# Kernel optimization log

Hardware: AMD Instinct MI355X
Metric: run time of the kernel (lower is better)

Reference implementation:

```python
import jax, jax.numpy as jnp
import numpy as np

B, C, H, W = 256, 3, 224, 224
RETINA = 32
NUM_ZOOM = 3
SCALE = 2
HG, HL = 1024, 256  # num_hidden_glimpse, num_hidden_location
GDIM = NUM_ZOOM * C * RETINA * RETINA  # 9216


def setup_inputs() -> dict:
    key = jax.random.key(0)
    ks = jax.random.split(key, 12)
    images = jax.random.normal(ks[0], (B, C, H, W), dtype=jnp.float32)
    # locations in [-0.4, 0.4] so all multi-scale crops are in-bounds
    locations = (jax.random.uniform(ks[1], (B, 2), dtype=jnp.float32) * 2.0 - 1.0) * 0.4
    def lin(kw, kb, fan_in, fan_out):
        s = 1.0 / np.sqrt(fan_in)
        Wm = jax.random.uniform(kw, (fan_in, fan_out), jnp.float32, -s, s)
        bm = jax.random.uniform(kb, (fan_out,), jnp.float32, -s, s)
        return Wm, bm
    W1, b1 = lin(ks[2], ks[3], GDIM, HG)
    W2, b2 = lin(ks[4], ks[5], 2, HL)
    W3, b3 = lin(ks[6], ks[7], HG, HG + HL)
    W4, b4 = lin(ks[8], ks[9], HL, HG + HL)
    return {"images": images, "locations": locations,
            "W1": W1, "b1": b1, "W2": W2, "b2": b2,
            "W3": W3, "b3": b3, "W4": W4, "b4": b4}


def _foveate(images, locations):
    # images (B,C,H,W); locations (B,2) in [-1,1]
    denorm = (locations + 1.0) * 0.5 * W  # denormalized pixel coords (row, col)
    zoom_patches = []
    for i in range(NUM_ZOOM):
        half = int(RETINA * 0.5 * SCALE ** i)
        size = 2 * half
        def crop(img, loc):
            # int() truncation == floor for in-bounds (non-negative) offsets
            top = jnp.trunc(loc[0] - half).astype(jnp.int32)
            left = jnp.trunc(loc[1] - half).astype(jnp.int32)
            return jax.lax.dynamic_slice(img, (jnp.int32(0), top, left), (C, size, size))
        crops = jax.vmap(crop)(images, denorm)  # (B,C,size,size)
        resized = jax.image.resize(crops, (crops.shape[0], C, RETINA, RETINA),
                                   method="bilinear", antialias=False)
        zoom_patches.append(resized)
    g = jnp.stack(zoom_patches, axis=1)  # (B, Z, C, r, r)
    return g.reshape(g.shape[0], -1)  # (B, Z*C*r*r)


def reference(images, locations, W1, b1, W2, b2, W3, b3, W4, b4):
    g = _foveate(images, locations)
    hg = jax.nn.relu(jax.nn.relu(g @ W1 + b1) @ W3 + b3)
    hl = jax.nn.relu(jax.nn.relu(locations @ W2 + b2) @ W4 + b4)
    return jax.nn.relu(hg + hl)
```

## Files before the change

kernel.cpp:

```cpp
#include <hip/hip_runtime.h>

typedef __attribute__((ext_vector_type(8))) short short8;
typedef __attribute__((ext_vector_type(16))) float f32x16;

#define Bsz 256
#define Cch 3
#define Him 224
#define Wim 224
#define RET 32
#define HG 1024
#define HL 256
#define GDIM 9216
#define NOUT 1280

__device__ __forceinline__ unsigned short f2bf(float x) {
  unsigned u = __float_as_uint(x);
  return (unsigned short)((u + 0x7fffu + ((u >> 16) & 1u)) >> 16);
}
__device__ __forceinline__ float bf2f(unsigned short h) {
  return __uint_as_float((unsigned)h << 16);
}

__global__ __launch_bounds__(256) void foveate_kernel(
    const float* __restrict__ img, const float* __restrict__ loc,
    unsigned short* __restrict__ ghi, unsigned short* __restrict__ glo) {
  int idx = blockIdx.x * 256 + threadIdx.x;
  int b = idx / GDIM;
  int r = idx - b * GDIM;
  int z = r / (Cch * RET * RET);
  int r2 = r - z * (Cch * RET * RET);
  int c = r2 / (RET * RET);
  int p = r2 - c * (RET * RET);
  int i = p >> 5, j = p & 31;
  float dr = (loc[b * 2 + 0] + 1.f) * .5f * (float)Wim;
  float dc = (loc[b * 2 + 1] + 1.f) * .5f * (float)Wim;
  int half = 16 << z;
  int top = (int)truncf(dr - (float)half), left = (int)truncf(dc - (float)half);
  const float* base = img + ((long)b * Cch + c) * (Him * Wim);
  float v;
  if (z == 0) {
    v = base[(top + i) * Wim + left + j];
  } else {
    int rr = (z == 1) ? top + 2 * i : top + 4 * i + 1;
    int cc = (z == 1) ? left + 2 * j : left + 4 * j + 1;
    v = .25f * (base[rr * Wim + cc] + base[rr * Wim + cc + 1] +
                base[(rr + 1) * Wim + cc] + base[(rr + 1) * Wim + cc + 1]);
  }
  unsigned short h = f2bf(v);
  ghi[idx] = h;
  glo[idx] = f2bf(v - bf2f(h));
}

__device__ __forceinline__ void gemm_block(
    const unsigned short* __restrict__ Ahi, const unsigned short* __restrict__ Alo,
    int lda, const float* __restrict__ Bf, int ldb,
    int m0, int n0, int kb, int iters,
    f32x16 acc[2][2], unsigned short* __restrict__ ldsA, float* __restrict__ ldsB) {
  const int t = threadIdx.x;
  const int lane = t & 63;
  const int wm = t >> 7, wn = (t >> 6) & 1;
  const int l5 = lane & 31, lh = lane >> 5;

  const unsigned short* aSrc[4];
  const float* bSrc[4];
  int aDst[4], bDst[4];
#pragma unroll
  for (int p = 0; p < 4; ++p) {
    int s = p * 256 + t;
    int m5 = s & 31, kseg = (s >> 5) & 3, mf = (s >> 7) & 3;
    const unsigned short* base = (s >> 9) ? Alo : Ahi;
    aSrc[p] = base + (long)(m0 + mf * 32 + m5) * lda + kb + kseg * 8;
    aDst[p] = s * 8;
    bSrc[p] = Bf + (long)(kb + (s & 1023) / 32) * ldb + n0 + (s & 31) * 4;
    bDst[p] = ((s & 1023) >> 5) * 128 + (s & 31) * 4;
  }

  for (int it = 0; it < iters; ++it) {
    uint4 av[4];
    float4 bv[4];
#pragma unroll
    for (int p = 0; p < 4; ++p) {
      av[p] = *(const uint4*)(aSrc[p] + it * 32);
      bv[p] = *(const float4*)(bSrc[p] + (long)it * 32 * ldb);
    }
    __syncthreads();
#pragma unroll
    for (int p = 0; p < 4; ++p) {
      *(uint4*)(ldsA + aDst[p]) = av[p];
      *(float4*)(ldsB + bDst[p]) = bv[p];
    }
    __syncthreads();
#pragma unroll
    for (int ks = 0; ks < 2; ++ks) {
      short8 ah[2], al[2], bh[2], bl[2];
#pragma unroll
      for (int mi = 0; mi < 2; ++mi) {
        int mf = wm * 2 + mi;
        int slot = mf * 128 + (ks * 2 + lh) * 32 + l5;
        ah[mi] = *(const short8*)(ldsA + slot * 8);
        al[mi] = *(const short8*)(ldsA + (slot + 512) * 8);
      }
#pragma unroll
      for (int ni = 0; ni < 2; ++ni) {
        int n = wn * 64 + ni * 32 + l5;
        int k0 = ks * 16 + lh * 8;
        short8 hh, ll;
#pragma unroll
        for (int j = 0; j < 8; ++j) {
          float v = ldsB[(k0 + j) * 128 + n];
          unsigned short h = f2bf(v);
          hh[j] = (short)h;
          ll[j] = (short)f2bf(v - bf2f(h));
        }
        bh[ni] = hh;
        bl[ni] = ll;
      }
#pragma unroll
      for (int mi = 0; mi < 2; ++mi)
#pragma unroll
        for (int ni = 0; ni < 2; ++ni) {
          acc[mi][ni] = __builtin_amdgcn_mfma_f32_32x32x16_bf16(ah[mi], bh[ni], acc[mi][ni], 0, 0, 0);
          acc[mi][ni] = __builtin_amdgcn_mfma_f32_32x32x16_bf16(ah[mi], bl[ni], acc[mi][ni], 0, 0, 0);
          acc[mi][ni] = __builtin_amdgcn_mfma_f32_32x32x16_bf16(al[mi], bh[ni], acc[mi][ni], 0, 0, 0);
        }
    }
  }
}

__device__ __forceinline__ void epilogue(float* __restrict__ Pz, int ldp, int m0,
                                         int n0, f32x16 acc[2][2]) {
  const int t = threadIdx.x, lane = t & 63;
  const int wm = t >> 7, wn = (t >> 6) & 1;
  const int l5 = lane & 31, lh = lane >> 5;
#pragma unroll
  for (int mi = 0; mi < 2; ++mi)
#pragma unroll
    for (int ni = 0; ni < 2; ++ni) {
      int col = n0 + wn * 64 + ni * 32 + l5;
      int rbase = m0 + wm * 64 + mi * 32 + 4 * lh;
#pragma unroll
      for (int r = 0; r < 16; ++r) {
        int row = rbase + (r & 3) + 8 * (r >> 2);
        Pz[(long)row * ldp + col] = acc[mi][ni][r];
      }
    }
}

__global__ __launch_bounds__(256, 2) void gemm1_kernel(
    const unsigned short* __restrict__ ghi, const unsigned short* __restrict__ glo,
    const float* __restrict__ W1, float* __restrict__ P) {
  __shared__ __align__(16) unsigned short ldsA[8192];
  __shared__ __align__(16) float ldsB[4096];
  f32x16 zz = {0, 0, 0, 0, 0, 0, 0, 0, 0, 0, 0, 0, 0, 0, 0, 0};
  f32x16 acc[2][2] = {zz, zz, zz, zz};
  int n0 = blockIdx.x * 128, m0 = blockIdx.y * 128, z = blockIdx.z;
  gemm_block(ghi, glo, GDIM, W1, HG, m0, n0, z * 288, 9, acc, ldsA, ldsB);
  epilogue(P + (long)z * Bsz * HG, HG, m0, n0, acc);
}

__global__ __launch_bounds__(256, 2) void gemm2_kernel(
    const unsigned short* __restrict__ h1hi, const unsigned short* __restrict__ h1lo,
    const unsigned short* __restrict__ h2hi, const unsigned short* __restrict__ h2lo,
    const float* __restrict__ W3, const float* __restrict__ W4,
    float* __restrict__ P) {
  __shared__ __align__(16) unsigned short ldsA[8192];
  __shared__ __align__(16) float ldsB[4096];
  f32x16 zz = {0, 0, 0, 0, 0, 0, 0, 0, 0, 0, 0, 0, 0, 0, 0, 0};
  f32x16 acc[2][2] = {zz, zz, zz, zz};
  int n0 = blockIdx.x * 128, m0 = blockIdx.y * 128, z = blockIdx.z;
  if (z < 8)
    gemm_block(h1hi, h1lo, HG, W3, NOUT, m0, n0, z * 128, 4, acc, ldsA, ldsB);
  else
    gemm_block(h2hi, h2lo, HL, W4, NOUT, m0, n0, (z - 8) * 128, 4, acc, ldsA, ldsB);
  epilogue(P + (long)z * Bsz * NOUT, NOUT, m0, n0, acc);
}

__global__ __launch_bounds__(256) void reduce1_h2_kernel(
    const float* __restrict__ P, const float* __restrict__ b1,
    const float* __restrict__ loc, const float* __restrict__ W2,
    const float* __restrict__ b2,
    unsigned short* __restrict__ h1hi, unsigned short* __restrict__ h1lo,
    unsigned short* __restrict__ h2hi, unsigned short* __restrict__ h2lo) {
  if (blockIdx.x < 256) {
    int i4 = (blockIdx.x * 256 + threadIdx.x) * 4;
    float4 s = *(const float4*)(P + i4);
    for (int z = 1; z < 32; ++z) {
      float4 p = *(const float4*)(P + (long)z * (Bsz * HG) + i4);
      s.x += p.x; s.y += p.y; s.z += p.z; s.w += p.w;
    }
    int n = i4 & (HG - 1);
    float4 bb = *(const float4*)(b1 + n);
    float v0 = fmaxf(s.x + bb.x, 0.f), v1 = fmaxf(s.y + bb.y, 0.f);
    float v2 = fmaxf(s.z + bb.z, 0.f), v3 = fmaxf(s.w + bb.w, 0.f);
    unsigned short h0 = f2bf(v0), h1 = f2bf(v1), h2 = f2bf(v2), h3 = f2bf(v3);
    *(ushort4*)(h1hi + i4) = make_ushort4(h0, h1, h2, h3);
    *(ushort4*)(h1lo + i4) = make_ushort4(f2bf(v0 - bf2f(h0)), f2bf(v1 - bf2f(h1)),
                                          f2bf(v2 - bf2f(h2)), f2bf(v3 - bf2f(h3)));
  } else {
    int i4 = ((blockIdx.x - 256) * 256 + threadIdx.x) * 4;
    int b = i4 >> 8, n = i4 & (HL - 1);
    float l0 = loc[b * 2 + 0], l1 = loc[b * 2 + 1];
    float4 w0 = *(const float4*)(W2 + n);
    float4 w1 = *(const float4*)(W2 + HL + n);
    float4 bb = *(const float4*)(b2 + n);
    float v0 = fmaxf(fmaf(l0, w0.x, fmaf(l1, w1.x, bb.x)), 0.f);
    float v1 = fmaxf(fmaf(l0, w0.y, fmaf(l1, w1.y, bb.y)), 0.f);
    float v2 = fmaxf(fmaf(l0, w0.z, fmaf(l1, w1.z, bb.z)), 0.f);
    float v3 = fmaxf(fmaf(l0, w0.w, fmaf(l1, w1.w, bb.w)), 0.f);
    unsigned short h0 = f2bf(v0), h1 = f2bf(v1), h2 = f2bf(v2), h3 = f2bf(v3);
    *(ushort4*)(h2hi + i4) = make_ushort4(h0, h1, h2, h3);
    *(ushort4*)(h2lo + i4) = make_ushort4(f2bf(v0 - bf2f(h0)), f2bf(v1 - bf2f(h1)),
                                          f2bf(v2 - bf2f(h2)), f2bf(v3 - bf2f(h3)));
  }
}

__global__ __launch_bounds__(256) void reduce2_kernel(
    const float* __restrict__ P, const float* __restrict__ b3,
    const float* __restrict__ b4, float* __restrict__ out) {
  int i4 = (blockIdx.x * 256 + threadIdx.x) * 4;
  float4 a = *(const float4*)(P + i4);
  for (int z = 1; z < 8; ++z) {
    float4 p = *(const float4*)(P + (long)z * (Bsz * NOUT) + i4);
    a.x += p.x; a.y += p.y; a.z += p.z; a.w += p.w;
  }
  float4 c8 = *(const float4*)(P + 8L * (Bsz * NOUT) + i4);
  float4 c9 = *(const float4*)(P + 9L * (Bsz * NOUT) + i4);
  int n = i4 % NOUT;
  float4 b3v = *(const float4*)(b3 + n);
  float4 b4v = *(const float4*)(b4 + n);
  float4 o;
  o.x = fmaxf(fmaxf(a.x + b3v.x, 0.f) + fmaxf(c8.x + c9.x + b4v.x, 0.f), 0.f);
  o.y = fmaxf(fmaxf(a.y + b3v.y, 0.f) + fmaxf(c8.y + c9.y + b4v.y, 0.f), 0.f);
  o.z = fmaxf(fmaxf(a.z + b3v.z, 0.f) + fmaxf(c8.z + c9.z + b4v.z, 0.f), 0.f);
  o.w = fmaxf(fmaxf(a.w + b3v.w, 0.f) + fmaxf(c8.w + c9.w + b4v.w, 0.f), 0.f);
  *(float4*)(out + i4) = o;
}

extern "C" void kernel_launch(void* const* d_in, const int* in_sizes, int n_in,
                              void* d_out, int out_size, void* d_ws, size_t ws_size,
                              hipStream_t stream) {
  const float* images = (const float*)d_in[0];
  const float* locs = (const float*)d_in[1];
  const float* W1 = (const float*)d_in[2];
  const float* b1 = (const float*)d_in[3];
  const float* W2 = (const float*)d_in[4];
  const float* b2 = (const float*)d_in[5];
  const float* W3 = (const float*)d_in[6];
  const float* b3 = (const float*)d_in[7];
  const float* W4 = (const float*)d_in[8];
  const float* b4 = (const float*)d_in[9];
  float* out = (float*)d_out;

  unsigned short* ghi = (unsigned short*)d_ws;
  unsigned short* glo = ghi + (long)Bsz * GDIM;
  unsigned short* h1hi = glo + (long)Bsz * GDIM;
  unsigned short* h1lo = h1hi + (long)Bsz * HG;
  unsigned short* h2hi = h1lo + (long)Bsz * HG;
  unsigned short* h2lo = h2hi + (long)Bsz * HL;
  float* P1 = (float*)(h2lo + (long)Bsz * HL);
  float* P2 = P1 + 32L * Bsz * HG;

  foveate_kernel<<<(Bsz * GDIM) / 256, 256, 0, stream>>>(images, locs, ghi, glo);
  gemm1_kernel<<<dim3(HG / 128, Bsz / 128, 32), 256, 0, stream>>>(ghi, glo, W1, P1);
  reduce1_h2_kernel<<<320, 256, 0, stream>>>(P1, b1, locs, W2, b2, h1hi, h1lo, h2hi, h2lo);
  gemm2_kernel<<<dim3(NOUT / 128, Bsz / 128, 10), 256, 0, stream>>>(
      h1hi, h1lo, h2hi, h2lo, W3, W4, P2);
  reduce2_kernel<<<(Bsz * NOUT) / 1024, 256, 0, stream>>>(P2, b3, b4, out);
}
```

Before: 343.8 us.

## Pre-split weights to bf16 hi/lo in k-blocked layout and retile GEMMs

```diff
diff --git a/kernel.cpp b/kernel.cpp
--- a/kernel.cpp
+++ b/kernel.cpp
@@ -47,97 +47,145 @@
                 base[(rr + 1) * Wim + cc] + base[(rr + 1) * Wim + cc + 1]);
   }
   unsigned short h = f2bf(v);
-  ghi[idx] = h;
-  glo[idx] = f2bf(v - bf2f(h));
-}
-
-__device__ __forceinline__ void gemm_block(
+  int off = (r >> 3) * 2048 + b * 8 + (r & 7);
+  ghi[off] = h;
+  glo[off] = f2bf(v - bf2f(h));
+}
+
+__global__ __launch_bounds__(256) void tconv_kernel(
+    const float* __restrict__ in, unsigned short* __restrict__ oh,
+    unsigned short* __restrict__ ol, int K, int N) {
+  __shared__ float tile[32][33];
+  int n0 = blockIdx.x * 32, k0 = blockIdx.y * 32;
+  int r = threadIdx.x >> 3, c4 = (threadIdx.x & 7) * 4;
+  float4 v = *(const float4*)(in + (long)(k0 + r) * N + n0 + c4);
+  tile[r][c4 + 0] = v.x; tile[r][c4 + 1] = v.y;
+  tile[r][c4 + 2] = v.z; tile[r][c4 + 3] = v.w;
+  __syncthreads();
+  if (threadIdx.x < 128) {
+    int rr = threadIdx.x >> 2, c8 = (threadIdx.x & 3) * 8;
+    unsigned hi01 = 0, hi23 = 0, hi45 = 0, hi67 = 0;
+    unsigned lo01 = 0, lo23 = 0, lo45 = 0, lo67 = 0;
+    unsigned hh[8], ll[8];
+#pragma unroll
+    for (int j = 0; j < 8; ++j) {
+      float x = tile[c8 + j][rr];
+      hh[j] = f2bf(x);
+      ll[j] = f2bf(x - bf2f((unsigned short)hh[j]));
+    }
+    hi01 = hh[0] | (hh[1] << 16); hi23 = hh[2] | (hh[3] << 16);
+    hi45 = hh[4] | (hh[5] << 16); hi67 = hh[6] | (hh[7] << 16);
+    lo01 = ll[0] | (ll[1] << 16); lo23 = ll[2] | (ll[3] << 16);
+    lo45 = ll[4] | (ll[5] << 16); lo67 = ll[6] | (ll[7] << 16);
+    long off = (long)((k0 + c8) >> 3) * (N * 8) + (n0 + rr) * 8;
+    *(uint4*)(oh + off) = make_uint4(hi01, hi23, hi45, hi67);
+    *(uint4*)(ol + off) = make_uint4(lo01, lo23, lo45, lo67);
+  }
+}
+
+__device__ __forceinline__ void gemm_core(
     const unsigned short* __restrict__ Ahi, const unsigned short* __restrict__ Alo,
-    int lda, const float* __restrict__ Bf, int ldb,
-    int m0, int n0, int kb, int iters,
-    f32x16 acc[2][2], unsigned short* __restrict__ ldsA, float* __restrict__ ldsB) {
-  const int t = threadIdx.x;
-  const int lane = t & 63;
-  const int wm = t >> 7, wn = (t >> 6) & 1;
+    const unsigned short* __restrict__ Bhi, const unsigned short* __restrict__ Blo,
+    int Bn, int n0, int kblk0, int iters, f32x16 acc[2][4],
+    unsigned short* __restrict__ lds) {
+  const int t = threadIdx.x, w = t >> 6, lane = t & 63;
   const int l5 = lane & 31, lh = lane >> 5;
-
-  const unsigned short* aSrc[4];
-  const float* bSrc[4];
-  int aDst[4], bDst[4];
-#pragma unroll
-  for (int p = 0; p < 4; ++p) {
-    int s = p * 256 + t;
-    int m5 = s & 31, kseg = (s >> 5) & 3, mf = (s >> 7) & 3;
-    const unsigned short* base = (s >> 9) ? Alo : Ahi;
-    aSrc[p] = base + (long)(m0 + mf * 32 + m5) * lda + kb + kseg * 8;
-    aDst[p] = s * 8;
-    bSrc[p] = Bf + (long)(kb + (s & 1023) / 32) * ldb + n0 + (s & 31) * 4;
-    bDst[p] = ((s & 1023) >> 5) * 128 + (s & 31) * 4;
+  unsigned short* lAh = lds;
+  unsigned short* lAl = lds + 8192;
+  unsigned short* lBh = lds + 16384;
+  unsigned short* lBl = lds + 20480;
+
+  uint4 rAh[4], rAl[4], rBh[2], rBl[2];
+  long aoff[4], boff[2];
+#pragma unroll
+  for (int q = 0; q < 4; ++q) aoff[q] = (long)kblk0 * 2048 + (q * 256 + t) * 8;
+#pragma unroll
+  for (int q = 0; q < 2; ++q) {
+    int s = q * 256 + t;
+    boff[q] = ((long)kblk0 + (s >> 7)) * Bn * 8 + (long)(n0 + (s & 127)) * 8;
+  }
+#pragma unroll
+  for (int q = 0; q < 4; ++q) {
+    rAh[q] = *(const uint4*)(Ahi + aoff[q]);
+    rAl[q] = *(const uint4*)(Alo + aoff[q]);
+  }
+#pragma unroll
+  for (int q = 0; q < 2; ++q) {
+    rBh[q] = *(const uint4*)(Bhi + boff[q]);
+    rBl[q] = *(const uint4*)(Blo + boff[q]);
   }
 
   for (int it = 0; it < iters; ++it) {
-    uint4 av[4];
-    float4 bv[4];
-#pragma unroll
-    for (int p = 0; p < 4; ++p) {
-      av[p] = *(const uint4*)(aSrc[p] + it * 32);
-      bv[p] = *(const float4*)(bSrc[p] + (long)it * 32 * ldb);
-    }
     __syncthreads();
 #pragma unroll
-    for (int p = 0; p < 4; ++p) {
-      *(uint4*)(ldsA + aDst[p]) = av[p];
-      *(float4*)(ldsB + bDst[p]) = bv[p];
+    for (int q = 0; q < 4; ++q) {
+      *(uint4*)(lAh + (q * 256 + t) * 8) = rAh[q];
+      *(uint4*)(lAl + (q * 256 + t) * 8) = rAl[q];
+    }
+#pragma unroll
+    for (int q = 0; q < 2; ++q) {
+      *(uint4*)(lBh + (q * 256 + t) * 8) = rBh[q];
+      *(uint4*)(lBl + (q * 256 + t) * 8) = rBl[q];
     }
     __syncthreads();
+    if (it + 1 < iters) {
+      long ka = (long)(it + 1) * 8192;
+      long kb = (long)(it + 1) * 4 * Bn * 8;
+#pragma unroll
+      for (int q = 0; q < 4; ++q) {
+        rAh[q] = *(const uint4*)(Ahi + aoff[q] + ka);
+        rAl[q] = *(const uint4*)(Alo + aoff[q] + ka);
+      }
+#pragma unroll
+      for (int q = 0; q < 2; ++q) {
+        rBh[q] = *(const uint4*)(Bhi + boff[q] + kb);
+        rBl[q] = *(const uint4*)(Blo + boff[q] + kb);
+      }
+    }
 #pragma unroll
     for (int ks = 0; ks < 2; ++ks) {
-      short8 ah[2], al[2], bh[2], bl[2];
+      short8 fa[2][2], fb[2][4];
 #pragma unroll
       for (int mi = 0; mi < 2; ++mi) {
-        int mf = wm * 2 + mi;
-        int slot = mf * 128 + (ks * 2 + lh) * 32 + l5;
-        ah[mi] = *(const short8*)(ldsA + slot * 8);
-        al[mi] = *(const short8*)(ldsA + (slot + 512) * 8);
-      }
-#pragma unroll
-      for (int ni = 0; ni < 2; ++ni) {
-        int n = wn * 64 + ni * 32 + l5;
-        int k0 = ks * 16 + lh * 8;
-        short8 hh, ll;
-#pragma unroll
-        for (int j = 0; j < 8; ++j) {
-          float v = ldsB[(k0 + j) * 128 + n];
-          unsigned short h = f2bf(v);
-          hh[j] = (short)h;
-          ll[j] = (short)f2bf(v - bf2f(h));
-        }
-        bh[ni] = hh;
-        bl[ni] = ll;
+        int off = ((ks * 2 + lh) * 256 + w * 64 + mi * 32 + l5) * 8;
+        fa[0][mi] = *(const short8*)(lAh + off);
+        fa[1][mi] = *(const short8*)(lAl + off);
+      }
+#pragma unroll
+      for (int ni = 0; ni < 4; ++ni) {
+        int off = ((ks * 2 + lh) * 128 + ni * 32 + l5) * 8;
+        fb[0][ni] = *(const short8*)(lBh + off);
+        fb[1][ni] = *(const short8*)(lBl + off);
       }
 #pragma unroll
       for (int mi = 0; mi < 2; ++mi)
 #pragma unroll
-        for (int ni = 0; ni < 2; ++ni) {
-          acc[mi][ni] = __builtin_amdgcn_mfma_f32_32x32x16_bf16(ah[mi], bh[ni], acc[mi][ni], 0, 0, 0);
-          acc[mi][ni] = __builtin_amdgcn_mfma_f32_32x32x16_bf16(ah[mi], bl[ni], acc[mi][ni], 0, 0, 0);
-          acc[mi][ni] = __builtin_amdgcn_mfma_f32_32x32x16_bf16(al[mi], bh[ni], acc[mi][ni], 0, 0, 0);
-        }
-    }
-  }
-}
-
-__device__ __forceinline__ void epilogue(float* __restrict__ Pz, int ldp, int m0,
-                                         int n0, f32x16 acc[2][2]) {
-  const int t = threadIdx.x, lane = t & 63;
-  const int wm = t >> 7, wn = (t >> 6) & 1;
+        for (int ni = 0; ni < 4; ++ni)
+          acc[mi][ni] = __builtin_amdgcn_mfma_f32_32x32x16_bf16(fa[0][mi], fb[0][ni], acc[mi][ni], 0, 0, 0);
+#pragma unroll
+      for (int mi = 0; mi < 2; ++mi)
+#pragma unroll
+        for (int ni = 0; ni < 4; ++ni)
+          acc[mi][ni] = __builtin_amdgcn_mfma_f32_32x32x16_bf16(fa[0][mi], fb[1][ni], acc[mi][ni], 0, 0, 0);
+#pragma unroll
+      for (int mi = 0; mi < 2; ++mi)
+#pragma unroll
+        for (int ni = 0; ni < 4; ++ni)
+          acc[mi][ni] = __builtin_amdgcn_mfma_f32_32x32x16_bf16(fa[1][mi], fb[0][ni], acc[mi][ni], 0, 0, 0);
+    }
+  }
+}
+
+__device__ __forceinline__ void epilogue(float* __restrict__ Pz, int ldp, int n0,
+                                         f32x16 acc[2][4]) {
+  const int t = threadIdx.x, w = t >> 6, lane = t & 63;
   const int l5 = lane & 31, lh = lane >> 5;
 #pragma unroll
   for (int mi = 0; mi < 2; ++mi)
 #pragma unroll
-    for (int ni = 0; ni < 2; ++ni) {
-      int col = n0 + wn * 64 + ni * 32 + l5;
-      int rbase = m0 + wm * 64 + mi * 32 + 4 * lh;
+    for (int ni = 0; ni < 4; ++ni) {
+      int col = n0 + ni * 32 + l5;
+      int rbase = w * 64 + mi * 32 + 4 * lh;
 #pragma unroll
       for (int r = 0; r < 16; ++r) {
         int row = rbase + (r & 3) + 8 * (r >> 2);
@@ -146,33 +194,43 @@
     }
 }
 
-__global__ __launch_bounds__(256, 2) void gemm1_kernel(
+__global__ __launch_bounds__(256, 1) void gemm1_kernel(
     const unsigned short* __restrict__ ghi, const unsigned short* __restrict__ glo,
-    const float* __restrict__ W1, float* __restrict__ P) {
-  __shared__ __align__(16) unsigned short ldsA[8192];
-  __shared__ __align__(16) float ldsB[4096];
-  f32x16 zz = {0, 0, 0, 0, 0, 0, 0, 0, 0, 0, 0, 0, 0, 0, 0, 0};
-  f32x16 acc[2][2] = {zz, zz, zz, zz};
-  int n0 = blockIdx.x * 128, m0 = blockIdx.y * 128, z = blockIdx.z;
-  gemm_block(ghi, glo, GDIM, W1, HG, m0, n0, z * 288, 9, acc, ldsA, ldsB);
-  epilogue(P + (long)z * Bsz * HG, HG, m0, n0, acc);
-}
-
-__global__ __launch_bounds__(256, 2) void gemm2_kernel(
+    const unsigned short* __restrict__ w1hi, const unsigned short* __restrict__ w1lo,
+    float* __restrict__ P) {
+  __shared__ __align__(16) unsigned short lds[24576];
+  f32x16 acc[2][4];
+#pragma unroll
+  for (int i = 0; i < 2; ++i)
+#pragma unroll
+    for (int j = 0; j < 4; ++j)
+#pragma unroll
+      for (int r = 0; r < 16; ++r) acc[i][j][r] = 0.f;
+  int n0 = blockIdx.x * 128, z = blockIdx.y;
+  gemm_core(ghi, glo, w1hi, w1lo, HG, n0, z * 36, 9, acc, lds);
+  epilogue(P + (long)z * Bsz * HG, HG, n0, acc);
+}
+
+__global__ __launch_bounds__(256, 1) void gemm2_kernel(
     const unsigned short* __restrict__ h1hi, const unsigned short* __restrict__ h1lo,
     const unsigned short* __restrict__ h2hi, const unsigned short* __restrict__ h2lo,
-    const float* __restrict__ W3, const float* __restrict__ W4,
+    const unsigned short* __restrict__ w3hi, const unsigned short* __restrict__ w3lo,
+    const unsigned short* __restrict__ w4hi, const unsigned short* __restrict__ w4lo,
     float* __restrict__ P) {
-  __shared__ __align__(16) unsigned short ldsA[8192];
-  __shared__ __align__(16) float ldsB[4096];
-  f32x16 zz = {0, 0, 0, 0, 0, 0, 0, 0, 0, 0, 0, 0, 0, 0, 0, 0};
-  f32x16 acc[2][2] = {zz, zz, zz, zz};
-  int n0 = blockIdx.x * 128, m0 = blockIdx.y * 128, z = blockIdx.z;
+  __shared__ __align__(16) unsigned short lds[24576];
+  f32x16 acc[2][4];
+#pragma unroll
+  for (int i = 0; i < 2; ++i)
+#pragma unroll
+    for (int j = 0; j < 4; ++j)
+#pragma unroll
+      for (int r = 0; r < 16; ++r) acc[i][j][r] = 0.f;
+  int n0 = blockIdx.x * 128, z = blockIdx.y;
   if (z < 8)
-    gemm_block(h1hi, h1lo, HG, W3, NOUT, m0, n0, z * 128, 4, acc, ldsA, ldsB);
+    gemm_core(h1hi, h1lo, w3hi, w3lo, NOUT, n0, z * 16, 4, acc, lds);
   else
-    gemm_block(h2hi, h2lo, HL, W4, NOUT, m0, n0, (z - 8) * 128, 4, acc, ldsA, ldsB);
-  epilogue(P + (long)z * Bsz * NOUT, NOUT, m0, n0, acc);
+    gemm_core(h2hi, h2lo, w4hi, w4lo, NOUT, n0, (z - 8) * 16, 4, acc, lds);
+  epilogue(P + (long)z * Bsz * NOUT, NOUT, n0, acc);
 }
 
 __global__ __launch_bounds__(256) void reduce1_h2_kernel(
@@ -188,29 +246,31 @@
       float4 p = *(const float4*)(P + (long)z * (Bsz * HG) + i4);
       s.x += p.x; s.y += p.y; s.z += p.z; s.w += p.w;
     }
-    int n = i4 & (HG - 1);
-    float4 bb = *(const float4*)(b1 + n);
+    int m = i4 >> 10, k = i4 & (HG - 1);
+    float4 bb = *(const float4*)(b1 + k);
     float v0 = fmaxf(s.x + bb.x, 0.f), v1 = fmaxf(s.y + bb.y, 0.f);
     float v2 = fmaxf(s.z + bb.z, 0.f), v3 = fmaxf(s.w + bb.w, 0.f);
     unsigned short h0 = f2bf(v0), h1 = f2bf(v1), h2 = f2bf(v2), h3 = f2bf(v3);
-    *(ushort4*)(h1hi + i4) = make_ushort4(h0, h1, h2, h3);
-    *(ushort4*)(h1lo + i4) = make_ushort4(f2bf(v0 - bf2f(h0)), f2bf(v1 - bf2f(h1)),
-                                          f2bf(v2 - bf2f(h2)), f2bf(v3 - bf2f(h3)));
+    int off = (k >> 3) * 2048 + m * 8 + (k & 7);
+    *(ushort4*)(h1hi + off) = make_ushort4(h0, h1, h2, h3);
+    *(ushort4*)(h1lo + off) = make_ushort4(f2bf(v0 - bf2f(h0)), f2bf(v1 - bf2f(h1)),
+                                           f2bf(v2 - bf2f(h2)), f2bf(v3 - bf2f(h3)));
   } else {
     int i4 = ((blockIdx.x - 256) * 256 + threadIdx.x) * 4;
-    int b = i4 >> 8, n = i4 & (HL - 1);
+    int b = i4 >> 8, k = i4 & (HL - 1);
     float l0 = loc[b * 2 + 0], l1 = loc[b * 2 + 1];
-    float4 w0 = *(const float4*)(W2 + n);
-    float4 w1 = *(const float4*)(W2 + HL + n);
-    float4 bb = *(const float4*)(b2 + n);
+    float4 w0 = *(const float4*)(W2 + k);
+    float4 w1 = *(const float4*)(W2 + HL + k);
+    float4 bb = *(const float4*)(b2 + k);
     float v0 = fmaxf(fmaf(l0, w0.x, fmaf(l1, w1.x, bb.x)), 0.f);
     float v1 = fmaxf(fmaf(l0, w0.y, fmaf(l1, w1.y, bb.y)), 0.f);
     float v2 = fmaxf(fmaf(l0, w0.z, fmaf(l1, w1.z, bb.z)), 0.f);
     float v3 = fmaxf(fmaf(l0, w0.w, fmaf(l1, w1.w, bb.w)), 0.f);
     unsigned short h0 = f2bf(v0), h1 = f2bf(v1), h2 = f2bf(v2), h3 = f2bf(v3);
-    *(ushort4*)(h2hi + i4) = make_ushort4(h0, h1, h2, h3);
-    *(ushort4*)(h2lo + i4) = make_ushort4(f2bf(v0 - bf2f(h0)), f2bf(v1 - bf2f(h1)),
-                                          f2bf(v2 - bf2f(h2)), f2bf(v3 - bf2f(h3)));
+    int off = (k >> 3) * 2048 + b * 8 + (k & 7);
+    *(ushort4*)(h2hi + off) = make_ushort4(h0, h1, h2, h3);
+    *(ushort4*)(h2lo + off) = make_ushort4(f2bf(v0 - bf2f(h0)), f2bf(v1 - bf2f(h1)),
+                                           f2bf(v2 - bf2f(h2)), f2bf(v3 - bf2f(h3)));
   }
 }
 
@@ -251,19 +311,28 @@
   const float* b4 = (const float*)d_in[9];
   float* out = (float*)d_out;
 
-  unsigned short* ghi = (unsigned short*)d_ws;
-  unsigned short* glo = ghi + (long)Bsz * GDIM;
-  unsigned short* h1hi = glo + (long)Bsz * GDIM;
-  unsigned short* h1lo = h1hi + (long)Bsz * HG;
-  unsigned short* h2hi = h1lo + (long)Bsz * HG;
-  unsigned short* h2lo = h2hi + (long)Bsz * HL;
-  float* P1 = (float*)(h2lo + (long)Bsz * HL);
-  float* P2 = P1 + 32L * Bsz * HG;
-
-  foveate_kernel<<<(Bsz * GDIM) / 256, 256, 0, stream>>>(images, locs, ghi, glo);
-  gemm1_kernel<<<dim3(HG / 128, Bsz / 128, 32), 256, 0, stream>>>(ghi, glo, W1, P1);
-  reduce1_h2_kernel<<<320, 256, 0, stream>>>(P1, b1, locs, W2, b2, h1hi, h1lo, h2hi, h2lo);
-  gemm2_kernel<<<dim3(NOUT / 128, Bsz / 128, 10), 256, 0, stream>>>(
-      h1hi, h1lo, h2hi, h2lo, W3, W4, P2);
+  unsigned short* p = (unsigned short*)d_ws;
+  unsigned short* gsh = p; p += 2359296;
+  unsigned short* gsl = p; p += 2359296;
+  unsigned short* w1h = p; p += 9437184;
+  unsigned short* w1l = p; p += 9437184;
+  unsigned short* w3h = p; p += 1310720;
+  unsigned short* w3l = p; p += 1310720;
+  unsigned short* w4h = p; p += 327680;
+  unsigned short* w4l = p; p += 327680;
+  unsigned short* h1h = p; p += 262144;
+  unsigned short* h1l = p; p += 262144;
+  unsigned short* h2h = p; p += 65536;
+  unsigned short* h2l = p; p += 65536;
+  float* P1 = (float*)p;
+  float* P2 = P1 + 8388608;
+
+  tconv_kernel<<<dim3(HG / 32, GDIM / 32), 256, 0, stream>>>(W1, w1h, w1l, GDIM, HG);
+  tconv_kernel<<<dim3(NOUT / 32, HG / 32), 256, 0, stream>>>(W3, w3h, w3l, HG, NOUT);
+  tconv_kernel<<<dim3(NOUT / 32, HL / 32), 256, 0, stream>>>(W4, w4h, w4l, HL, NOUT);
+  foveate_kernel<<<(Bsz * GDIM) / 256, 256, 0, stream>>>(images, locs, gsh, gsl);
+  gemm1_kernel<<<dim3(8, 32), 256, 0, stream>>>(gsh, gsl, w1h, w1l, P1);
+  reduce1_h2_kernel<<<320, 256, 0, stream>>>(P1, b1, locs, W2, b2, h1h, h1l, h2h, h2l);
+  gemm2_kernel<<<dim3(10, 10), 256, 0, stream>>>(h1h, h1l, h2h, h2l, w3h, w3l, w4h, w4l, P2);
   reduce2_kernel<<<(Bsz * NOUT) / 1024, 256, 0, stream>>>(P2, b3, b4, out);
 }
```

Result: faster. 330.4 us (-3.9%).
